# Performance work log

Hardware: AMD Instinct MI355X
Metric: run time of the kernel (lower is better)

The kernel has to match this reference:

```python
import jax, jax.numpy as jnp
import numpy as np

N_NODES = 100000
N_EDGES = 1600000
IN_FEATS = 128
N_HIDDEN = 128
N_CLASSES = 47


def setup_inputs() -> dict:
    key = jax.random.key(0)
    ks = jax.random.split(key, 9)
    x = jax.random.normal(ks[0], (N_NODES, IN_FEATS), dtype=jnp.float32)
    src = jax.random.randint(ks[1], (N_EDGES,), 0, N_NODES, dtype=jnp.int32)
    dst = jax.random.randint(ks[2], (N_EDGES,), 0, N_NODES, dtype=jnp.int32)
    s = 0.05
    return {
        "x": x, "src": src, "dst": dst,
        "Ws0": jax.random.normal(ks[3], (IN_FEATS, N_HIDDEN), jnp.float32) * s,
        "Wn0": jax.random.normal(ks[4], (IN_FEATS, N_HIDDEN), jnp.float32) * s,
        "b0": jnp.zeros((N_HIDDEN,), jnp.float32),
        "Ws1": jax.random.normal(ks[5], (N_HIDDEN, N_HIDDEN), jnp.float32) * s,
        "Wn1": jax.random.normal(ks[6], (N_HIDDEN, N_HIDDEN), jnp.float32) * s,
        "b1": jnp.zeros((N_HIDDEN,), jnp.float32),
        "Ws2": jax.random.normal(ks[7], (N_HIDDEN, N_CLASSES), jnp.float32) * s,
        "Wn2": jax.random.normal(ks[8], (N_HIDDEN, N_CLASSES), jnp.float32) * s,
        "b2": jnp.zeros((N_CLASSES,), jnp.float32),
    }


def _sage_layer(h, src, dst, inv_deg, Ws, Wn, b):
    # weighted (w=1) mean aggregation over in-neighbors: sum(h[src]) / in_degree
    msg = h[src]  # [E, d] irregular gather
    neigh = jax.ops.segment_sum(msg, dst, num_segments=N_NODES) * inv_deg[:, None]
    # DGL SAGEConv 'mean': fc_self(h_self) + fc_neigh(h_neigh), bias on self branch
    return h @ Ws + neigh @ Wn + b


def reference(x, src, dst, Ws0, Wn0, b0, Ws1, Wn1, b1, Ws2, Wn2, b2):
    deg = jax.ops.segment_sum(jnp.ones_like(dst, dtype=x.dtype), dst, num_segments=N_NODES)
    inv_deg = 1.0 / jnp.maximum(deg, 1.0)
    h = _sage_layer(x, src, dst, inv_deg, Ws0, Wn0, b0)
    h = jax.nn.relu(h)  # dropout is identity (eval / p=0)
    h = _sage_layer(h, src, dst, inv_deg, Ws1, Wn1, b1)
    h = jax.nn.relu(h)
    h = _sage_layer(h, src, dst, inv_deg, Ws2, Wn2, b2)
    return jax.nn.log_softmax(h, axis=-1)
```

## Files before the change

### kernel.cpp

```cpp
#include <hip/hip_runtime.h>
#include <hip/hip_bf16.h>

#define NN 100000
#define NE 1600000
#define F 128
#define NCLS 47

#define SCAN_B 98
#define NPB 256
#define BUCKETS 391
#define ABLK 512
#define ACHUNK (NE / ABLK)

typedef __attribute__((ext_vector_type(8))) short short8;
typedef __attribute__((ext_vector_type(8))) unsigned short u16x8;
typedef __attribute__((ext_vector_type(4))) float f32x4;

#define MFMA16(A, B, C) __builtin_amdgcn_mfma_f32_16x16x32_bf16(A, B, C, 0, 0, 0)

__device__ __forceinline__ unsigned short b16(float f) {
    unsigned int u = __builtin_bit_cast(unsigned int, f);
    unsigned int r = u + 0x7FFFu + ((u >> 16) & 1u);
    return (unsigned short)(r >> 16);
}
__device__ __forceinline__ float bflo(unsigned int u) { return __builtin_bit_cast(float, u << 16); }
__device__ __forceinline__ float bfhi(unsigned int u) { return __builtin_bit_cast(float, u & 0xFFFF0000u); }

__global__ void __launch_bounds__(256) k_bhist(const int* __restrict__ dst,
                                               int* __restrict__ bucket_cnt) {
    __shared__ int hist[BUCKETS];
    const int t = threadIdx.x;
    for (int i = t; i < BUCKETS; i += 256) hist[i] = 0;
    __syncthreads();
    const int e0 = blockIdx.x * ACHUNK;
    for (int i = t; i < ACHUNK; i += 256) atomicAdd(&hist[dst[e0 + i] >> 8], 1);
    __syncthreads();
    for (int i = t; i < BUCKETS; i += 256)
        if (hist[i]) atomicAdd(&bucket_cnt[i], hist[i]);
}

__global__ void k_bscan(const int* __restrict__ bucket_cnt, int* __restrict__ bucket_off,
                        int* __restrict__ cursor) {
    const int lane = threadIdx.x & 63;
    int run = 0;
#pragma unroll
    for (int c = 0; c < 7; c++) {
        int idx = c * 64 + lane;
        int v = (idx < BUCKETS) ? bucket_cnt[idx] : 0;
        int s = v;
#pragma unroll
        for (int off = 1; off < 64; off <<= 1) {
            int n = __shfl_up(s, off);
            if (lane >= off) s += n;
        }
        int excl = run + s - v;
        if (idx <= BUCKETS) {
            bucket_off[idx] = excl;
            cursor[idx] = excl;
        }
        run += __shfl(s, 63);
    }
}

__global__ void __launch_bounds__(256) k_bscatter(const int* __restrict__ src,
                                                  const int* __restrict__ dst,
                                                  int* __restrict__ cursor,
                                                  int2* __restrict__ ebuf) {
    __shared__ int hist[BUCKETS];
    __shared__ int base[BUCKETS];
    __shared__ int rank[BUCKETS];
    const int t = threadIdx.x;
    for (int i = t; i < BUCKETS; i += 256) {
        hist[i] = 0;
        rank[i] = 0;
    }
    __syncthreads();
    const int e0 = blockIdx.x * ACHUNK;
    for (int i = t; i < ACHUNK; i += 256) atomicAdd(&hist[dst[e0 + i] >> 8], 1);
    __syncthreads();
    for (int i = t; i < BUCKETS; i += 256) {
        int h = hist[i];
        base[i] = h ? atomicAdd(&cursor[i], h) : 0;
    }
    __syncthreads();
    for (int i = t; i < ACHUNK; i += 256) {
        int s = src[e0 + i];
        int d = dst[e0 + i];
        int b = d >> 8;
        int r = atomicAdd(&rank[b], 1);
        ebuf[base[b] + r] = make_int2(s, d);
    }
}

__global__ void __launch_bounds__(256) k_bdeg(const int2* __restrict__ ebuf,
                                              const int* __restrict__ bucket_off,
                                              int* __restrict__ deg) {
    __shared__ int cnt[NPB];
    const int t = threadIdx.x;
    cnt[t] = 0;
    __syncthreads();
    const int e0 = bucket_off[blockIdx.x], e1 = bucket_off[blockIdx.x + 1];
    for (int i = e0 + t; i < e1; i += 256) atomicAdd(&cnt[ebuf[i].y & 255], 1);
    __syncthreads();
    int node = (blockIdx.x << 8) + t;
    if (node < NN) deg[node] = cnt[t];
}

__global__ void __launch_bounds__(256) k_bfill(const int2* __restrict__ ebuf,
                                               const int* __restrict__ bucket_off,
                                               const int* __restrict__ row_off,
                                               int* __restrict__ col) {
    __shared__ int ro[NPB];
    __shared__ int cur[NPB];
    const int t = threadIdx.x;
    int node = (blockIdx.x << 8) + t;
    ro[t] = (node < NN) ? row_off[node] : 0;
    cur[t] = 0;
    __syncthreads();
    const int e0 = bucket_off[blockIdx.x], e1 = bucket_off[blockIdx.x + 1];
    for (int i = e0 + t; i < e1; i += 256) {
        int2 e = ebuf[i];
        int d = e.y & 255;
        int p = atomicAdd(&cur[d], 1);
        col[ro[d] + p] = e.x;
    }
}

__global__ void __launch_bounds__(256) k_part(const int* __restrict__ deg,
                                              int* __restrict__ partials) {
    __shared__ int ws[4];
    const int t = threadIdx.x, lane = t & 63, wid = t >> 6;
    int i0 = blockIdx.x * 1024 + t * 4;
    int s = 0;
    if (i0 + 3 < NN) {
        int4 v = *(const int4*)&deg[i0];
        s = v.x + v.y + v.z + v.w;
    } else {
#pragma unroll
        for (int j = 0; j < 4; j++) {
            int idx = i0 + j;
            if (idx < NN) s += deg[idx];
        }
    }
#pragma unroll
    for (int off = 1; off < 64; off <<= 1) s += __shfl_xor(s, off);
    if (lane == 0) ws[wid] = s;
    __syncthreads();
    if (t == 0) partials[blockIdx.x] = ws[0] + ws[1] + ws[2] + ws[3];
}

__global__ void k_scanpart(int* __restrict__ partials, int* __restrict__ row_off) {
    const int lane = threadIdx.x & 63;
    int v0 = (lane < SCAN_B) ? partials[lane] : 0;
    int i1 = lane + 64;
    int v1 = (i1 < SCAN_B) ? partials[i1] : 0;
    int s0 = v0;
#pragma unroll
    for (int off = 1; off < 64; off <<= 1) {
        int n = __shfl_up(s0, off);
        if (lane >= off) s0 += n;
    }
    int tot0 = __shfl(s0, 63);
    int s1 = v1;
#pragma unroll
    for (int off = 1; off < 64; off <<= 1) {
        int n = __shfl_up(s1, off);
        if (lane >= off) s1 += n;
    }
    if (lane < SCAN_B) partials[lane] = s0 - v0;
    if (i1 < SCAN_B) partials[i1] = tot0 + s1 - v1;
    if (lane == 0) row_off[NN] = NE;
}

__global__ void __launch_bounds__(256) k_offsets(const int* __restrict__ deg,
                                                 const int* __restrict__ partials,
                                                 int* __restrict__ row_off,
                                                 float* __restrict__ inv_deg) {
    __shared__ int wsum[4];
    const int t = threadIdx.x, lane = t & 63, wid = t >> 6;
    int i0 = blockIdx.x * 1024 + t * 4;
    int v[4];
    int loc = 0;
#pragma unroll
    for (int j = 0; j < 4; j++) {
        int idx = i0 + j;
        v[j] = (idx < NN) ? deg[idx] : 0;
        loc += v[j];
    }
    int run = loc;
#pragma unroll
    for (int off = 1; off < 64; off <<= 1) {
        int n = __shfl_up(run, off);
        if (lane >= off) run += n;
    }
    if (lane == 63) wsum[wid] = run;
    __syncthreads();
    int woff = partials[blockIdx.x];
#pragma unroll
    for (int wv = 0; wv < 4; wv++)
        if (wv < wid) woff += wsum[wv];
    int excl = woff + run - loc;
#pragma unroll
    for (int j = 0; j < 4; j++) {
        int idx = i0 + j;
        if (idx < NN) {
            row_off[idx] = excl;
            inv_deg[idx] = 1.0f / fmaxf((float)v[j], 1.0f);
            excl += v[j];
        }
    }
}

__global__ void k_cvt(const float* __restrict__ x, unsigned short* __restrict__ xb) {
    int t = blockIdx.x * blockDim.x + threadIdx.x;
    if (t >= NN * F / 8) return;
    const float4* x4 = (const float4*)x;
    float4 a = x4[t * 2], b = x4[t * 2 + 1];
    u16x8 o;
    o[0] = b16(a.x); o[1] = b16(a.y); o[2] = b16(a.z); o[3] = b16(a.w);
    o[4] = b16(b.x); o[5] = b16(b.y); o[6] = b16(b.z); o[7] = b16(b.w);
    ((u16x8*)xb)[t] = o;
}

__global__ void k_pack_all(const float* __restrict__ Ws0, const float* __restrict__ Wn0,
                           const float* __restrict__ Ws1, const float* __restrict__ Wn1,
                           const float* __restrict__ Ws2, const float* __restrict__ Wn2,
                           unsigned short* __restrict__ wp) {
    int idx = blockIdx.x * blockDim.x + threadIdx.x;
    if (idx >= 77824) return;
    const float* W;
    int base, ncols;
    if (idx < 65536) {
        int m = idx >> 14;
        W = (m == 0) ? Ws0 : (m == 1) ? Wn0 : (m == 2) ? Ws1 : Wn1;
        base = m << 14;
        ncols = 128;
    } else {
        int m = (idx - 65536) / 6144;
        W = m ? Wn2 : Ws2;
        base = 65536 + m * 6144;
        ncols = NCLS;
    }
    int li = idx - base;
    int nt = li >> 11;
    int r = li & 2047;
    int kk = r >> 9;
    int r2 = r & 511;
    int lane = r2 >> 3;
    int j = r2 & 7;
    int k = kk * 32 + ((lane >> 4) << 3) + j;
    int n = nt * 16 + (lane & 15);
    float v = (n < ncols) ? W[k * ncols + n] : 0.f;
    wp[idx] = b16(v);
}

__global__ void __launch_bounds__(256) k_aggb(const unsigned int* __restrict__ hb32,
                                              const int* __restrict__ row_off,
                                              const int* __restrict__ col,
                                              const float* __restrict__ inv_deg,
                                              unsigned int* __restrict__ ab32) {
    int node = (blockIdx.x * blockDim.x + threadIdx.x) >> 6;
    int lane = threadIdx.x & 63;
    if (node >= NN) return;
    int b = row_off[node], e = row_off[node + 1];
    int deg = e - b;
    float ax = 0.f, ay = 0.f;
    const unsigned int* hp = hb32 + lane;
    for (int base = 0; base < deg; base += 64) {
        int cnt = deg - base;
        if (cnt > 64) cnt = 64;
        int myc = col[b + base + (lane < cnt ? lane : 0)];
        for (int jj = 0; jj < cnt; jj += 16) {
            int cs[16];
            unsigned int us[16];
#pragma unroll
            for (int k = 0; k < 16; k++) {
                int idx = jj + k;
                cs[k] = __shfl(myc, idx < cnt ? idx : 0);
            }
#pragma unroll
            for (int k = 0; k < 16; k++) us[k] = hp[(unsigned)cs[k] * 64u];
#pragma unroll
            for (int k = 0; k < 16; k++) {
                if (jj + k < cnt) {
                    ax += bflo(us[k]);
                    ay += bfhi(us[k]);
                }
            }
        }
    }
    float s = inv_deg[node];
    ax *= s; ay *= s;
    ab32[(size_t)node * 64 + lane] = (unsigned int)b16(ax) | ((unsigned int)b16(ay) << 16);
}

template <bool RELU>
__global__ void __launch_bounds__(256) k_layer(const unsigned short* __restrict__ hb,
                                               const unsigned short* __restrict__ ab,
                                               const unsigned short* __restrict__ wps,
                                               const unsigned short* __restrict__ wpn,
                                               const float* __restrict__ bias,
                                               unsigned short* __restrict__ outb) {
    const int wid = threadIdx.x >> 6, lane = threadIdx.x & 63;
    const int tile0 = blockIdx.x * 64;
    const short8* ws8 = (const short8*)wps;
    const short8* wn8 = (const short8*)wpn;
    short8 wf[2][2][4];
#pragma unroll
    for (int t = 0; t < 2; t++) {
        int nt = 2 * wid + t;
#pragma unroll
        for (int kk = 0; kk < 4; kk++) {
            wf[0][t][kk] = ws8[(nt * 4 + kk) * 64 + lane];
            wf[1][t][kk] = wn8[(nt * 4 + kk) * 64 + lane];
        }
    }
    const int rb = lane & 15, kq = lane >> 4;
    float bv[2];
#pragma unroll
    for (int t = 0; t < 2; t++) bv[t] = bias[(2 * wid + t) * 16 + rb];
    const short8* h8 = (const short8*)hb;
    const short8* a8 = (const short8*)ab;
    f32x4 zero = {0.f, 0.f, 0.f, 0.f};
    f32x4 acc[4][2];
#pragma unroll
    for (int m = 0; m < 4; m++)
#pragma unroll
        for (int t = 0; t < 2; t++) acc[m][t] = zero;
#pragma unroll
    for (int kk = 0; kk < 4; kk++) {
#pragma unroll
        for (int m = 0; m < 4; m++) {
            int row = tile0 + m * 16 + rb;
            int rc = row < NN ? row : NN - 1;
            int idx = rc * 16 + kk * 4 + kq;
            short8 af = h8[idx];
            short8 gf = a8[idx];
            acc[m][0] = MFMA16(af, wf[0][0][kk], acc[m][0]);
            acc[m][1] = MFMA16(af, wf[0][1][kk], acc[m][1]);
            acc[m][0] = MFMA16(gf, wf[1][0][kk], acc[m][0]);
            acc[m][1] = MFMA16(gf, wf[1][1][kk], acc[m][1]);
        }
    }
#pragma unroll
    for (int m = 0; m < 4; m++) {
#pragma unroll
        for (int reg = 0; reg < 4; reg++) {
            int row = tile0 + m * 16 + kq * 4 + reg;
            if (row < NN) {
#pragma unroll
                for (int t = 0; t < 2; t++) {
                    float v = acc[m][t][reg] + bv[t];
                    if (RELU) v = fmaxf(v, 0.f);
                    outb[(size_t)row * F + (2 * wid + t) * 16 + rb] = b16(v);
                }
            }
        }
    }
}

__global__ void __launch_bounds__(512) k_out(const unsigned short* __restrict__ hb,
                                             const unsigned short* __restrict__ ab,
                                             const unsigned short* __restrict__ wps,
                                             const unsigned short* __restrict__ wpn,
                                             const float* __restrict__ bias,
                                             float* __restrict__ out) {
    const int wid = threadIdx.x >> 6, lane = threadIdx.x & 63;
    const int R0 = blockIdx.x * 128 + wid * 16;
    const short8* ws8 = (const short8*)wps;
    const short8* wn8 = (const short8*)wpn;
    short8 wf[2][3][4];
#pragma unroll
    for (int nt = 0; nt < 3; nt++)
#pragma unroll
        for (int kk = 0; kk < 4; kk++) {
            wf[0][nt][kk] = ws8[(nt * 4 + kk) * 64 + lane];
            wf[1][nt][kk] = wn8[(nt * 4 + kk) * 64 + lane];
        }
    const int rb = lane & 15, kq = lane >> 4;
    float bv[3];
    bool valid[3];
#pragma unroll
    for (int nt = 0; nt < 3; nt++) {
        int c = nt * 16 + rb;
        valid[nt] = c < NCLS;
        bv[nt] = valid[nt] ? bias[c] : 0.f;
    }
    const short8* h8 = (const short8*)hb;
    const short8* a8 = (const short8*)ab;
    f32x4 zero = {0.f, 0.f, 0.f, 0.f};
    f32x4 acc[3] = {zero, zero, zero};
    int rowr = R0 + rb;
    int rc = rowr < NN ? rowr : NN - 1;
#pragma unroll
    for (int kk = 0; kk < 4; kk++) {
        int idx = rc * 16 + kk * 4 + kq;
        short8 af = h8[idx];
        short8 gf = a8[idx];
#pragma unroll
        for (int nt = 0; nt < 3; nt++) {
            acc[nt] = MFMA16(af, wf[0][nt][kk], acc[nt]);
            acc[nt] = MFMA16(gf, wf[1][nt][kk], acc[nt]);
        }
    }
#pragma unroll
    for (int reg = 0; reg < 4; reg++) {
        int row = R0 + kq * 4 + reg;
        float v[3];
        float mx = -1e30f;
#pragma unroll
        for (int nt = 0; nt < 3; nt++) {
            v[nt] = acc[nt][reg] + bv[nt];
            if (valid[nt]) mx = fmaxf(mx, v[nt]);
        }
        for (int off = 1; off < 16; off <<= 1) mx = fmaxf(mx, __shfl_xor(mx, off));
        float s = 0.f;
#pragma unroll
        for (int nt = 0; nt < 3; nt++)
            if (valid[nt]) s += expf(v[nt] - mx);
        for (int off = 1; off < 16; off <<= 1) s += __shfl_xor(s, off);
        float L = mx + logf(s);
        if (row < NN) {
#pragma unroll
            for (int nt = 0; nt < 3; nt++)
                if (valid[nt]) out[(size_t)row * NCLS + nt * 16 + rb] = v[nt] - L;
        }
    }
}

extern "C" void kernel_launch(void* const* d_in, const int* in_sizes, int n_in,
                              void* d_out, int out_size, void* d_ws, size_t ws_size,
                              hipStream_t stream) {
    (void)in_sizes; (void)n_in; (void)out_size; (void)ws_size;
    const float* x = (const float*)d_in[0];
    const int* src = (const int*)d_in[1];
    const int* dst = (const int*)d_in[2];
    const float* Ws0 = (const float*)d_in[3];
    const float* Wn0 = (const float*)d_in[4];
    const float* b0 = (const float*)d_in[5];
    const float* Ws1 = (const float*)d_in[6];
    const float* Wn1 = (const float*)d_in[7];
    const float* b1 = (const float*)d_in[8];
    const float* Ws2 = (const float*)d_in[9];
    const float* Wn2 = (const float*)d_in[10];
    const float* b2 = (const float*)d_in[11];
    float* out = (float*)d_out;

    char* w = (char*)d_ws;
    size_t off = 0;
    auto alloc = [&](size_t bytes) -> char* {
        char* p = w + off;
        off = (off + bytes + 255) & ~(size_t)255;
        return p;
    };
    int* deg = (int*)alloc((size_t)NN * 4);
    int* row_off = (int*)alloc((size_t)(NN + 1) * 4);
    int* col = (int*)alloc((size_t)NE * 4);
    float* inv_deg = (float*)alloc((size_t)NN * 4);
    int* partials = (int*)alloc((size_t)SCAN_B * 4);
    int* bucket_cnt = (int*)alloc((size_t)(BUCKETS + 1) * 4);
    int* bucket_off = (int*)alloc((size_t)(BUCKETS + 1) * 4);
    int* bcursor = (int*)alloc((size_t)(BUCKETS + 1) * 4);
    int2* ebuf = (int2*)alloc((size_t)NE * 8);
    unsigned short* xb = (unsigned short*)alloc((size_t)NN * F * 2);
    unsigned short* aggb = (unsigned short*)alloc((size_t)NN * F * 2);
    unsigned short* h1b = (unsigned short*)alloc((size_t)NN * F * 2);
    unsigned short* h2b = (unsigned short*)alloc((size_t)NN * F * 2);
    unsigned short* wp = (unsigned short*)alloc((size_t)77824 * 2);

    hipMemsetAsync(bucket_cnt, 0, (size_t)(BUCKETS + 1) * 4, stream);

    k_bhist<<<ABLK, 256, 0, stream>>>(dst, bucket_cnt);
    k_bscan<<<1, 64, 0, stream>>>(bucket_cnt, bucket_off, bcursor);
    k_bscatter<<<ABLK, 256, 0, stream>>>(src, dst, bcursor, ebuf);
    k_bdeg<<<BUCKETS, 256, 0, stream>>>(ebuf, bucket_off, deg);
    k_part<<<SCAN_B, 256, 0, stream>>>(deg, partials);
    k_scanpart<<<1, 64, 0, stream>>>(partials, row_off);
    k_offsets<<<SCAN_B, 256, 0, stream>>>(deg, partials, row_off, inv_deg);
    k_bfill<<<BUCKETS, 256, 0, stream>>>(ebuf, bucket_off, row_off, col);

    k_cvt<<<(NN * F / 8 + 255) / 256, 256, 0, stream>>>(x, xb);
    k_pack_all<<<(77824 + 255) / 256, 256, 0, stream>>>(Ws0, Wn0, Ws1, Wn1, Ws2, Wn2, wp);

    unsigned short* wS0 = wp;
    unsigned short* wN0 = wp + 16384;
    unsigned short* wS1 = wp + 32768;
    unsigned short* wN1 = wp + 49152;
    unsigned short* wS2 = wp + 65536;
    unsigned short* wN2 = wp + 71680;

    const int AGG_B = NN * 64 / 256;
    const int LYR_B = (NN + 63) / 64;
    const int OUT_B = (NN + 127) / 128;

    k_aggb<<<AGG_B, 256, 0, stream>>>((const unsigned int*)xb, row_off, col, inv_deg,
                                      (unsigned int*)aggb);
    k_layer<true><<<LYR_B, 256, 0, stream>>>(xb, aggb, wS0, wN0, b0, h1b);
    k_aggb<<<AGG_B, 256, 0, stream>>>((const unsigned int*)h1b, row_off, col, inv_deg,
                                      (unsigned int*)aggb);
    k_layer<true><<<LYR_B, 256, 0, stream>>>(h1b, aggb, wS1, wN1, b1, h2b);
    k_aggb<<<AGG_B, 256, 0, stream>>>((const unsigned int*)h2b, row_off, col, inv_deg,
                                      (unsigned int*)aggb);
    k_out<<<OUT_B, 512, 0, stream>>>(h2b, aggb, wS2, wN2, b2, out);
}
```

Measured before the change: 355.2 us.

## Project before aggregating in last layer and widen gather loads to 16 bytes

The last layer now multiplies h2 by Wn2 first (128 to 47 columns, padded to 64) and aggregates the narrower projected features, so the final gather moves half the bytes. The neighbour sum stays in fp32 and is added inside the log-softmax kernel. The 128-wide aggregation kernel also switches from 4-byte to 16-byte gathers, with 4 edges processed in parallel per wave and a cross-lane reduction at the end. This adds one kernel launch and reuses the edge buffer as scratch, and it changes rounding slightly because the projection now happens before the mean.

```diff
diff --git a/kernel.cpp b/kernel.cpp
--- a/kernel.cpp
+++ b/kernel.cpp
@@ -254,44 +254,113 @@
     wp[idx] = b16(v);
 }
 
-__global__ void __launch_bounds__(256) k_aggb(const unsigned int* __restrict__ hb32,
+__global__ void __launch_bounds__(256) k_aggb(const uint4* __restrict__ h4,
                                               const int* __restrict__ row_off,
                                               const int* __restrict__ col,
                                               const float* __restrict__ inv_deg,
-                                              unsigned int* __restrict__ ab32) {
+                                              uint4* __restrict__ a4) {
     int node = (blockIdx.x * blockDim.x + threadIdx.x) >> 6;
     int lane = threadIdx.x & 63;
     if (node >= NN) return;
     int b = row_off[node], e = row_off[node + 1];
     int deg = e - b;
-    float ax = 0.f, ay = 0.f;
-    const unsigned int* hp = hb32 + lane;
+    const int g = lane >> 4, fl = lane & 15;
+    float acc[8];
+#pragma unroll
+    for (int i = 0; i < 8; i++) acc[i] = 0.f;
     for (int base = 0; base < deg; base += 64) {
         int cnt = deg - base;
         if (cnt > 64) cnt = 64;
         int myc = col[b + base + (lane < cnt ? lane : 0)];
         for (int jj = 0; jj < cnt; jj += 16) {
-            int cs[16];
-            unsigned int us[16];
-#pragma unroll
-            for (int k = 0; k < 16; k++) {
-                int idx = jj + k;
-                cs[k] = __shfl(myc, idx < cnt ? idx : 0);
+            uint4 u[4];
+#pragma unroll
+            for (int k2 = 0; k2 < 4; k2++) {
+                int r = jj + k2 * 4 + g;
+                int c = __shfl(myc, r < cnt ? r : 0);
+                u[k2] = h4[(size_t)(unsigned)c * 16u + fl];
             }
 #pragma unroll
-            for (int k = 0; k < 16; k++) us[k] = hp[(unsigned)cs[k] * 64u];
-#pragma unroll
-            for (int k = 0; k < 16; k++) {
-                if (jj + k < cnt) {
-                    ax += bflo(us[k]);
-                    ay += bfhi(us[k]);
-                }
+            for (int k2 = 0; k2 < 4; k2++) {
+                int r = jj + k2 * 4 + g;
+                unsigned m = (r < cnt) ? 0xFFFFFFFFu : 0u;
+                uint4 v = u[k2];
+                v.x &= m; v.y &= m; v.z &= m; v.w &= m;
+                acc[0] += bflo(v.x); acc[1] += bfhi(v.x);
+                acc[2] += bflo(v.y); acc[3] += bfhi(v.y);
+                acc[4] += bflo(v.z); acc[5] += bfhi(v.z);
+                acc[6] += bflo(v.w); acc[7] += bfhi(v.w);
             }
         }
     }
-    float s = inv_deg[node];
-    ax *= s; ay *= s;
-    ab32[(size_t)node * 64 + lane] = (unsigned int)b16(ax) | ((unsigned int)b16(ay) << 16);
+#pragma unroll
+    for (int i = 0; i < 8; i++) {
+        acc[i] += __shfl_xor(acc[i], 16);
+        acc[i] += __shfl_xor(acc[i], 32);
+    }
+    if (g == 0) {
+        float s = inv_deg[node];
+        uint4 o;
+        o.x = (unsigned)b16(acc[0] * s) | ((unsigned)b16(acc[1] * s) << 16);
+        o.y = (unsigned)b16(acc[2] * s) | ((unsigned)b16(acc[3] * s) << 16);
+        o.z = (unsigned)b16(acc[4] * s) | ((unsigned)b16(acc[5] * s) << 16);
+        o.w = (unsigned)b16(acc[6] * s) | ((unsigned)b16(acc[7] * s) << 16);
+        a4[(size_t)node * 16 + fl] = o;
+    }
+}
+
+__global__ void __launch_bounds__(256) k_agg48(const uint4* __restrict__ hw4,
+                                               const int* __restrict__ row_off,
+                                               const int* __restrict__ col,
+                                               const float* __restrict__ inv_deg,
+                                               float4* __restrict__ aggf4) {
+    int node = (blockIdx.x * blockDim.x + threadIdx.x) >> 6;
+    int lane = threadIdx.x & 63;
+    if (node >= NN) return;
+    int b = row_off[node], e = row_off[node + 1];
+    int deg = e - b;
+    const int g = lane >> 3, fl = lane & 7;
+    float acc[8];
+#pragma unroll
+    for (int i = 0; i < 8; i++) acc[i] = 0.f;
+    for (int base = 0; base < deg; base += 64) {
+        int cnt = deg - base;
+        if (cnt > 64) cnt = 64;
+        int myc = col[b + base + (lane < cnt ? lane : 0)];
+        for (int jj = 0; jj < cnt; jj += 16) {
+            uint4 u[2];
+#pragma unroll
+            for (int k2 = 0; k2 < 2; k2++) {
+                int r = jj + k2 * 8 + g;
+                int c = __shfl(myc, r < cnt ? r : 0);
+                u[k2] = hw4[(size_t)(unsigned)c * 8u + fl];
+            }
+#pragma unroll
+            for (int k2 = 0; k2 < 2; k2++) {
+                int r = jj + k2 * 8 + g;
+                unsigned m = (r < cnt) ? 0xFFFFFFFFu : 0u;
+                uint4 v = u[k2];
+                v.x &= m; v.y &= m; v.z &= m; v.w &= m;
+                acc[0] += bflo(v.x); acc[1] += bfhi(v.x);
+                acc[2] += bflo(v.y); acc[3] += bfhi(v.y);
+                acc[4] += bflo(v.z); acc[5] += bfhi(v.z);
+                acc[6] += bflo(v.w); acc[7] += bfhi(v.w);
+            }
+        }
+    }
+#pragma unroll
+    for (int i = 0; i < 8; i++) {
+        acc[i] += __shfl_xor(acc[i], 8);
+        acc[i] += __shfl_xor(acc[i], 16);
+        acc[i] += __shfl_xor(acc[i], 32);
+    }
+    if (lane < 8) {
+        float s = inv_deg[node];
+        float4 o0 = make_float4(acc[0] * s, acc[1] * s, acc[2] * s, acc[3] * s);
+        float4 o1 = make_float4(acc[4] * s, acc[5] * s, acc[6] * s, acc[7] * s);
+        aggf4[(size_t)node * 16 + fl * 2] = o0;
+        aggf4[(size_t)node * 16 + fl * 2 + 1] = o1;
+    }
 }
 
 template <bool RELU>
@@ -359,24 +428,53 @@
     }
 }
 
-__global__ void __launch_bounds__(512) k_out(const unsigned short* __restrict__ hb,
-                                             const unsigned short* __restrict__ ab,
-                                             const unsigned short* __restrict__ wps,
-                                             const unsigned short* __restrict__ wpn,
-                                             const float* __restrict__ bias,
-                                             float* __restrict__ out) {
+__global__ void __launch_bounds__(512) k_nmul(const unsigned short* __restrict__ hb,
+                                              const unsigned short* __restrict__ wpn,
+                                              unsigned short* __restrict__ hw) {
+    const int wid = threadIdx.x >> 6, lane = threadIdx.x & 63;
+    const int R0 = blockIdx.x * 128 + wid * 16;
+    const short8* wn8 = (const short8*)wpn;
+    short8 wf[3][4];
+#pragma unroll
+    for (int nt = 0; nt < 3; nt++)
+#pragma unroll
+        for (int kk = 0; kk < 4; kk++) wf[nt][kk] = wn8[(nt * 4 + kk) * 64 + lane];
+    const int rb = lane & 15, kq = lane >> 4;
+    const short8* h8 = (const short8*)hb;
+    f32x4 zero = {0.f, 0.f, 0.f, 0.f};
+    f32x4 acc[3] = {zero, zero, zero};
+    int rowr = R0 + rb;
+    int rc = rowr < NN ? rowr : NN - 1;
+#pragma unroll
+    for (int kk = 0; kk < 4; kk++) {
+        short8 af = h8[rc * 16 + kk * 4 + kq];
+#pragma unroll
+        for (int nt = 0; nt < 3; nt++) acc[nt] = MFMA16(af, wf[nt][kk], acc[nt]);
+    }
+#pragma unroll
+    for (int reg = 0; reg < 4; reg++) {
+        int row = R0 + kq * 4 + reg;
+        if (row < NN) {
+#pragma unroll
+            for (int nt = 0; nt < 3; nt++)
+                hw[(size_t)row * 64 + nt * 16 + rb] = b16(acc[nt][reg]);
+        }
+    }
+}
+
+__global__ void __launch_bounds__(512) k_out2(const unsigned short* __restrict__ hb,
+                                              const float* __restrict__ aggf,
+                                              const unsigned short* __restrict__ wps,
+                                              const float* __restrict__ bias,
+                                              float* __restrict__ out) {
     const int wid = threadIdx.x >> 6, lane = threadIdx.x & 63;
     const int R0 = blockIdx.x * 128 + wid * 16;
     const short8* ws8 = (const short8*)wps;
-    const short8* wn8 = (const short8*)wpn;
-    short8 wf[2][3][4];
+    short8 wf[3][4];
 #pragma unroll
     for (int nt = 0; nt < 3; nt++)
 #pragma unroll
-        for (int kk = 0; kk < 4; kk++) {
-            wf[0][nt][kk] = ws8[(nt * 4 + kk) * 64 + lane];
-            wf[1][nt][kk] = wn8[(nt * 4 + kk) * 64 + lane];
-        }
+        for (int kk = 0; kk < 4; kk++) wf[nt][kk] = ws8[(nt * 4 + kk) * 64 + lane];
     const int rb = lane & 15, kq = lane >> 4;
     float bv[3];
     bool valid[3];
@@ -387,30 +485,26 @@
         bv[nt] = valid[nt] ? bias[c] : 0.f;
     }
     const short8* h8 = (const short8*)hb;
-    const short8* a8 = (const short8*)ab;
     f32x4 zero = {0.f, 0.f, 0.f, 0.f};
     f32x4 acc[3] = {zero, zero, zero};
     int rowr = R0 + rb;
     int rc = rowr < NN ? rowr : NN - 1;
 #pragma unroll
     for (int kk = 0; kk < 4; kk++) {
-        int idx = rc * 16 + kk * 4 + kq;
-        short8 af = h8[idx];
-        short8 gf = a8[idx];
-#pragma unroll
-        for (int nt = 0; nt < 3; nt++) {
-            acc[nt] = MFMA16(af, wf[0][nt][kk], acc[nt]);
-            acc[nt] = MFMA16(gf, wf[1][nt][kk], acc[nt]);
-        }
+        short8 af = h8[rc * 16 + kk * 4 + kq];
+#pragma unroll
+        for (int nt = 0; nt < 3; nt++) acc[nt] = MFMA16(af, wf[nt][kk], acc[nt]);
     }
 #pragma unroll
     for (int reg = 0; reg < 4; reg++) {
         int row = R0 + kq * 4 + reg;
+        int rc2 = row < NN ? row : NN - 1;
         float v[3];
         float mx = -1e30f;
 #pragma unroll
         for (int nt = 0; nt < 3; nt++) {
-            v[nt] = acc[nt][reg] + bv[nt];
+            float av = aggf[(size_t)rc2 * 64 + nt * 16 + rb];
+            v[nt] = acc[nt][reg] + av + bv[nt];
             if (valid[nt]) mx = fmaxf(mx, v[nt]);
         }
         for (int off = 1; off < 16; off <<= 1) mx = fmaxf(mx, __shfl_xor(mx, off));
@@ -468,6 +562,9 @@
     unsigned short* h2b = (unsigned short*)alloc((size_t)NN * F * 2);
     unsigned short* wp = (unsigned short*)alloc((size_t)77824 * 2);
 
+    unsigned short* hw2b = (unsigned short*)ebuf;
+    float* agg2f = (float*)aggb;
+
     hipMemsetAsync(bucket_cnt, 0, (size_t)(BUCKETS + 1) * 4, stream);
 
     k_bhist<<<ABLK, 256, 0, stream>>>(dst, bucket_cnt);
@@ -493,13 +590,12 @@
     const int LYR_B = (NN + 63) / 64;
     const int OUT_B = (NN + 127) / 128;
 
-    k_aggb<<<AGG_B, 256, 0, stream>>>((const unsigned int*)xb, row_off, col, inv_deg,
-                                      (unsigned int*)aggb);
+    k_aggb<<<AGG_B, 256, 0, stream>>>((const uint4*)xb, row_off, col, inv_deg, (uint4*)aggb);
     k_layer<true><<<LYR_B, 256, 0, stream>>>(xb, aggb, wS0, wN0, b0, h1b);
-    k_aggb<<<AGG_B, 256, 0, stream>>>((const unsigned int*)h1b, row_off, col, inv_deg,
-                                      (unsigned int*)aggb);
+    k_aggb<<<AGG_B, 256, 0, stream>>>((const uint4*)h1b, row_off, col, inv_deg, (uint4*)aggb);
     k_layer<true><<<LYR_B, 256, 0, stream>>>(h1b, aggb, wS1, wN1, b1, h2b);
-    k_aggb<<<AGG_B, 256, 0, stream>>>((const unsigned int*)h2b, row_off, col, inv_deg,
-                                      (unsigned int*)aggb);
-    k_out<<<OUT_B, 512, 0, stream>>>(h2b, aggb, wS2, wN2, b2, out);
-}
+    k_nmul<<<OUT_B, 512, 0, stream>>>(h2b, wN2, hw2b);
+    k_agg48<<<AGG_B, 256, 0, stream>>>((const uint4*)hw2b, row_off, col, inv_deg,
+                                       (float4*)agg2f);
+    k_out2<<<OUT_B, 512, 0, stream>>>(h2b, agg2f, wS2, b2, out);
+}
```

Measured after the change: 334.0 us. -6.0%, faster.
